# Kernel tuning notes

Hardware: AMD Instinct MI355X
Metric: run time of the kernel (lower is better)

## Reference

```python
import jax, jax.numpy as jnp
import numpy as np

B, S, D, H = 2, 2048, 1024, 16
HD = D // H
NEG = -10000.0


def setup_inputs() -> dict:
    key = jax.random.key(0)
    ks = jax.random.split(key, 9)
    # xavier-uniform-like scale for square d_model x d_model weights
    lim = float(np.sqrt(6.0 / (D + D)))
    mk_w = lambda k: jax.random.uniform(k, (D, D), jnp.float32, -lim, lim)
    return {
        "q": jax.random.normal(ks[0], (B, S, D), jnp.float32),
        "k": jax.random.normal(ks[1], (B, S, D), jnp.float32),
        "v": jax.random.normal(ks[2], (B, S, D), jnp.float32),
        "attn_mask": jax.random.randint(ks[3], (B, S), 0, 2, jnp.int32),
        "Wq": mk_w(ks[4]),
        "Wk": mk_w(ks[5]),
        "Wv": mk_w(ks[6]),
        "Wo": mk_w(ks[7]),
        "mask_future": 1,
    }


def reference(q, k, v, attn_mask, Wq, Wk, Wv, Wo, mask_future):
    # nn.Linear(bias=False): y = x @ W.T
    def split_heads(x, W):
        return (x @ W.T).reshape(B, S, H, HD).transpose(0, 2, 1, 3)  # [B,H,S,HD]

    qh = split_heads(q, Wq)
    kh = split_heads(k, Wk)
    vh = split_heads(v, Wv)

    scale = 1.0 / np.sqrt(HD)
    scores = jnp.einsum("bhld,bhsd->bhls", qh, kh) * scale  # [B,H,L,S]

    if mask_future:  # static python flag
        rows = jnp.arange(S)[:, None]
        cols = jnp.arange(S)[None, :]
        causal_bias = jnp.where(cols > rows, jnp.float32(NEG), jnp.float32(0.0))
        scores = scores + causal_bias

    # masked_fill(attn_mask == 0, -10000): sets score exactly to NEG (after bias add)
    pad = attn_mask[:, None, None, :]  # [B,1,1,S]
    scores = jnp.where(pad == 0, jnp.float32(NEG), scores)

    probs = jax.nn.softmax(scores, axis=-1)
    ctx = jnp.einsum("bhls,bhsd->bhld", probs, vh)  # [B,H,L,HD]
    ctx = ctx.transpose(0, 2, 1, 3).reshape(B, S, D)
    return ctx @ Wo.T
```

## Files before the change

kernel.cpp:

```cpp
#include <hip/hip_runtime.h>
#include <hip/hip_bf16.h>

typedef __attribute__((ext_vector_type(8))) short bf16x8;
typedef __attribute__((ext_vector_type(4))) short bf16x4;
typedef __attribute__((ext_vector_type(4))) float f32x4;

#define B_ 2
#define S_ 2048
#define D_ 1024
#define H_ 16
#define HD_ 64
#define M_ 4096
#define NEGV (-10000.0f)

#define NQ_ 4194304
#define NW_ 1048576

#if __has_builtin(__builtin_amdgcn_mfma_f32_16x16x16bf16_1k)
#define HAVE_MFMA16 1
#else
#define HAVE_MFMA16 0
#endif

static __device__ __forceinline__ unsigned short f2bf(float x) {
  __hip_bfloat16 h = __float2bfloat16(x);
  return *reinterpret_cast<unsigned short*>(&h);
}

static __device__ __forceinline__ bf16x8 cvt8(const float* p) {
  float4 a = *reinterpret_cast<const float4*>(p);
  float4 b = *reinterpret_cast<const float4*>(p + 4);
  bf16x8 r;
  r[0] = (short)f2bf(a.x); r[1] = (short)f2bf(a.y);
  r[2] = (short)f2bf(a.z); r[3] = (short)f2bf(a.w);
  r[4] = (short)f2bf(b.x); r[5] = (short)f2bf(b.y);
  r[6] = (short)f2bf(b.z); r[7] = (short)f2bf(b.w);
  return r;
}

static __device__ __forceinline__ void gl_lds16(const unsigned short* g, unsigned short* l) {
#if __has_builtin(__builtin_amdgcn_global_load_lds)
  __builtin_amdgcn_global_load_lds(
      (const __attribute__((address_space(1))) unsigned int*)g,
      (__attribute__((address_space(3))) unsigned int*)l, 16, 0, 0);
#else
  *reinterpret_cast<bf16x8*>(l) = *reinterpret_cast<const bf16x8*>(g);
#endif
}


__global__ __launch_bounds__(256) void cvt_all(const float* __restrict__ q,
                                               const float* __restrict__ k,
                                               const float* __restrict__ v,
                                               const float* __restrict__ wq,
                                               const float* __restrict__ wk,
                                               const float* __restrict__ wv,
                                               const float* __restrict__ wo,
                                               unsigned short* __restrict__ dst) {
  for (size_t c = (size_t)blockIdx.x * 256 + threadIdx.x; c < 2097152; c += (size_t)2048 * 256) {
    const size_t e = c * 8;
    const float* s;
    if (e < (size_t)NQ_)            s = q  + e;
    else if (e < (size_t)2 * NQ_)   s = k  + (e - (size_t)NQ_);
    else if (e < (size_t)3 * NQ_)   s = v  + (e - (size_t)2 * NQ_);
    else if (e < (size_t)3 * NQ_ + NW_)     s = wq + (e - (size_t)3 * NQ_);
    else if (e < (size_t)3 * NQ_ + 2 * NW_) s = wk + (e - (size_t)3 * NQ_ - NW_);
    else if (e < (size_t)3 * NQ_ + 3 * NW_) s = wv + (e - (size_t)3 * NQ_ - 2 * NW_);
    else                                    s = wo + (e - (size_t)3 * NQ_ - 3 * NW_);
    *reinterpret_cast<bf16x8*>(dst + e) = cvt8(s);
  }
}

template<bool HSPLIT>
static __device__ __forceinline__ void core_fast(const unsigned short* A,
                                                 const unsigned short* Bw,
                                                 unsigned short* Asm, unsigned short* Bsm,
                                                 int m0, int n0, f32x4 (*acc)[4]) {
  const int tid = threadIdx.x, lane = tid & 63, wid = tid >> 6;
  const int wm = wid >> 1, wn = wid & 1;
  const int l15 = lane & 15, l4 = lane >> 4;

  for (int k0 = 0; k0 < 1024; k0 += 64) {
    __syncthreads();
#pragma unroll
    for (int i = 0; i < 4; ++i) {
      const int idx = tid + 256 * i;
      const int row = idx >> 3;
      const int ce = ((idx & 7) * 8) ^ ((row & 7) << 3);
      const unsigned short* ga;
      if constexpr (HSPLIT) {
        const int m = m0 + row, kk = k0 + ce;
        const int bb = m >> 11, s = m & 2047;
        ga = A + (((size_t)(bb * H_ + (kk >> 6)) * S_ + s) * HD_ + (kk & 63));
      } else {
        ga = A + (size_t)(m0 + row) * 1024 + k0 + ce;
      }
      gl_lds16(ga, Asm + (size_t)idx * 8);
      gl_lds16(Bw + (size_t)(n0 + row) * 1024 + k0 + ce, Bsm + (size_t)idx * 8);
    }
    __syncthreads();
#pragma unroll
    for (int kk = 0; kk < 2; ++kk) {
      bf16x8 af[4], bfr[4];
#pragma unroll
      for (int f = 0; f < 4; ++f) {
        const int ra = wm * 64 + f * 16 + l15;
        const int ca = (kk * 32 + l4 * 8) ^ ((ra & 7) << 3);
        af[f] = *reinterpret_cast<const bf16x8*>(&Asm[ra * 64 + ca]);
        const int rb = wn * 64 + f * 16 + l15;
        const int cb = (kk * 32 + l4 * 8) ^ ((rb & 7) << 3);
        bfr[f] = *reinterpret_cast<const bf16x8*>(&Bsm[rb * 64 + cb]);
      }
#pragma unroll
      for (int fm = 0; fm < 4; ++fm)
#pragma unroll
        for (int fn = 0; fn < 4; ++fn)
          acc[fm][fn] = __builtin_amdgcn_mfma_f32_16x16x32_bf16(af[fm], bfr[fn], acc[fm][fn], 0, 0, 0);
    }
  }
}

__global__ __launch_bounds__(256) void gemm_qkv_fast(const unsigned short* __restrict__ qbf,
                                                     const unsigned short* __restrict__ kbf,
                                                     const unsigned short* __restrict__ vbf,
                                                     const unsigned short* __restrict__ wbf,
                                                     unsigned short* __restrict__ Qh,
                                                     unsigned short* __restrict__ Kh,
                                                     unsigned short* __restrict__ Vt) {
  __shared__ unsigned short Asm[128 * 64];
  __shared__ unsigned short Bsm[128 * 64];
  const int z = blockIdx.z;
  const unsigned short* A  = (z == 0) ? qbf : (z == 1) ? kbf : vbf;
  const unsigned short* Bw = wbf + (size_t)z * NW_;
  const int m0 = blockIdx.y * 128, n0 = blockIdx.x * 128;
  const int lane = threadIdx.x & 63, wid = threadIdx.x >> 6;
  const int wm = wid >> 1, wn = wid & 1;
  const int l15 = lane & 15, l4 = lane >> 4;
  f32x4 acc[4][4] = {};
  core_fast<false>(A, Bw, Asm, Bsm, m0, n0, acc);

#pragma unroll
  for (int fm = 0; fm < 4; ++fm) {
#pragma unroll
    for (int fn = 0; fn < 4; ++fn) {
      const int mg0 = m0 + wm * 64 + fm * 16 + l4 * 4;
      const int ng  = n0 + wn * 64 + fn * 16 + l15;
      const int bidx = mg0 >> 11, s = mg0 & 2047;
      const int h = ng >> 6, d = ng & 63;
      if (z < 2) {
        unsigned short* C = (z == 0) ? Qh : Kh;
#pragma unroll
        for (int r = 0; r < 4; ++r)
          C[((size_t)((bidx * H_ + h) * S_ + s + r)) * HD_ + d] = f2bf(acc[fm][fn][r]);
      } else {
        ushort4 pk;
        pk.x = f2bf(acc[fm][fn][0]); pk.y = f2bf(acc[fm][fn][1]);
        pk.z = f2bf(acc[fm][fn][2]); pk.w = f2bf(acc[fm][fn][3]);
        *reinterpret_cast<ushort4*>(&Vt[((size_t)((bidx * H_ + h) * HD_ + d)) * S_ + s]) = pk;
      }
    }
  }
}

__global__ __launch_bounds__(256) void gemm_o_fast(const unsigned short* __restrict__ ctx,
                                                   const unsigned short* __restrict__ wobf,
                                                   float* __restrict__ Cout) {
  __shared__ unsigned short Asm[128 * 64];
  __shared__ unsigned short Bsm[128 * 64];
  const int m0 = blockIdx.y * 128, n0 = blockIdx.x * 128;
  const int lane = threadIdx.x & 63, wid = threadIdx.x >> 6;
  const int wm = wid >> 1, wn = wid & 1;
  const int l15 = lane & 15, l4 = lane >> 4;
  f32x4 acc[4][4] = {};
  core_fast<true>(ctx, wobf, Asm, Bsm, m0, n0, acc);

#pragma unroll
  for (int fm = 0; fm < 4; ++fm)
#pragma unroll
    for (int fn = 0; fn < 4; ++fn) {
      const int mg0 = m0 + wm * 64 + fm * 16 + l4 * 4;
      const int ng  = n0 + wn * 64 + fn * 16 + l15;
#pragma unroll
      for (int r = 0; r < 4; ++r)
        Cout[(size_t)(mg0 + r) * 1024 + ng] = acc[fm][fn][r];
    }
}


template<bool AF32, bool BF32, bool HSPLIT>
static __device__ __forceinline__ void gemm_core(const void* Av, const void* Bv,
                                                 unsigned short* Asm, unsigned short* Bsm,
                                                 int m0, int n0, f32x4 (*acc)[4]) {
  constexpr int BK = 64, LDT = 72;
  constexpr int K = 1024;
  const int tid = threadIdx.x;
  const int lane = tid & 63, wid = tid >> 6;
  const int wm = wid >> 1, wn = wid & 1;
  const int l15 = lane & 15, l4 = lane >> 4;

  for (int k0 = 0; k0 < K; k0 += BK) {
    __syncthreads();
#pragma unroll
    for (int i = 0; i < 4; ++i) {
      int idx = tid + 256 * i;
      int row = idx >> 3, k8 = (idx & 7) * 8;
      bf16x8 va, vb;
      if constexpr (AF32) {
        va = cvt8((const float*)Av + (size_t)(m0 + row) * K + k0 + k8);
      } else if constexpr (HSPLIT) {
        const int m = m0 + row, kk = k0 + k8;
        const int bb = m >> 11, s = m & 2047;
        va = *reinterpret_cast<const bf16x8*>(
            (const unsigned short*)Av +
            (((size_t)(bb * H_ + (kk >> 6)) * S_ + s) * HD_ + (kk & 63)));
      } else {
        va = *reinterpret_cast<const bf16x8*>((const unsigned short*)Av + (size_t)(m0 + row) * K + k0 + k8);
      }
      if constexpr (BF32) {
        vb = cvt8((const float*)Bv + (size_t)(n0 + row) * K + k0 + k8);
      } else {
        vb = *reinterpret_cast<const bf16x8*>((const unsigned short*)Bv + (size_t)(n0 + row) * K + k0 + k8);
      }
      *reinterpret_cast<bf16x8*>(&Asm[row * LDT + k8]) = va;
      *reinterpret_cast<bf16x8*>(&Bsm[row * LDT + k8]) = vb;
    }
    __syncthreads();
#pragma unroll
    for (int kk = 0; kk < 2; ++kk) {
      bf16x8 af[4], bfr[4];
#pragma unroll
      for (int f = 0; f < 4; ++f) {
        af[f]  = *reinterpret_cast<const bf16x8*>(&Asm[(wm * 64 + f * 16 + l15) * LDT + kk * 32 + l4 * 8]);
        bfr[f] = *reinterpret_cast<const bf16x8*>(&Bsm[(wn * 64 + f * 16 + l15) * LDT + kk * 32 + l4 * 8]);
      }
#pragma unroll
      for (int fm = 0; fm < 4; ++fm)
#pragma unroll
        for (int fn = 0; fn < 4; ++fn)
          acc[fm][fn] = __builtin_amdgcn_mfma_f32_16x16x32_bf16(af[fm], bfr[fn], acc[fm][fn], 0, 0, 0);
    }
  }
}

__global__ __launch_bounds__(256) void gemm_qkv3(const float* __restrict__ q,
                                                 const float* __restrict__ k,
                                                 const float* __restrict__ v,
                                                 const float* __restrict__ Wq,
                                                 const float* __restrict__ Wk,
                                                 const float* __restrict__ Wv,
                                                 unsigned short* __restrict__ Qh,
                                                 unsigned short* __restrict__ Kh,
                                                 unsigned short* __restrict__ Vt) {
  constexpr int LDT = 72;
  __shared__ unsigned short Asm[128 * LDT];
  __shared__ unsigned short Bsm[128 * LDT];
  const int z = blockIdx.z;
  const float* A  = (z == 0) ? q  : (z == 1) ? k  : v;
  const float* Bw = (z == 0) ? Wq : (z == 1) ? Wk : Wv;
  const int m0 = blockIdx.y * 128, n0 = blockIdx.x * 128;
  const int lane = threadIdx.x & 63, wid = threadIdx.x >> 6;
  const int wm = wid >> 1, wn = wid & 1;
  const int l15 = lane & 15, l4 = lane >> 4;
  f32x4 acc[4][4] = {};
  gemm_core<true, true, false>(A, Bw, Asm, Bsm, m0, n0, acc);

#pragma unroll
  for (int fm = 0; fm < 4; ++fm) {
#pragma unroll
    for (int fn = 0; fn < 4; ++fn) {
      const int mg0 = m0 + wm * 64 + fm * 16 + l4 * 4;
      const int ng  = n0 + wn * 64 + fn * 16 + l15;
      const int bidx = mg0 >> 11, s = mg0 & 2047;
      const int h = ng >> 6, d = ng & 63;
      if (z < 2) {
        unsigned short* C = (z == 0) ? Qh : Kh;
#pragma unroll
        for (int r = 0; r < 4; ++r)
          C[((size_t)((bidx * H_ + h) * S_ + s + r)) * HD_ + d] = f2bf(acc[fm][fn][r]);
      } else {
        ushort4 pk;
        pk.x = f2bf(acc[fm][fn][0]); pk.y = f2bf(acc[fm][fn][1]);
        pk.z = f2bf(acc[fm][fn][2]); pk.w = f2bf(acc[fm][fn][3]);
        *reinterpret_cast<ushort4*>(&Vt[((size_t)((bidx * H_ + h) * HD_ + d)) * S_ + s]) = pk;
      }
    }
  }
}

__global__ __launch_bounds__(256) void gemm_oproj(const void* __restrict__ Av,
                                                  const void* __restrict__ Bv,
                                                  float* __restrict__ Cout) {
  constexpr int LDT = 72;
  __shared__ unsigned short Asm[128 * LDT];
  __shared__ unsigned short Bsm[128 * LDT];
  const int m0 = blockIdx.y * 128, n0 = blockIdx.x * 128;
  const int lane = threadIdx.x & 63, wid = threadIdx.x >> 6;
  const int wm = wid >> 1, wn = wid & 1;
  const int l15 = lane & 15, l4 = lane >> 4;
  f32x4 acc[4][4] = {};
  gemm_core<false, true, true>(Av, Bv, Asm, Bsm, m0, n0, acc);

#pragma unroll
  for (int fm = 0; fm < 4; ++fm)
#pragma unroll
    for (int fn = 0; fn < 4; ++fn) {
      const int mg0 = m0 + wm * 64 + fm * 16 + l4 * 4;
      const int ng  = n0 + wn * 64 + fn * 16 + l15;
#pragma unroll
      for (int r = 0; r < 4; ++r)
        Cout[(size_t)(mg0 + r) * 1024 + ng] = acc[fm][fn][r];
    }
}

__global__ __launch_bounds__(128) void attn_fwd(const unsigned short* Qh,
                                                const unsigned short* __restrict__ Kh,
                                                const unsigned short* __restrict__ Vt,
                                                const int* __restrict__ attn_mask,
                                                const int* __restrict__ mask_future,
                                                unsigned short* ctx) {
  constexpr int KVB = 64;
  __shared__ unsigned short Ksm[64 * 64];
  __shared__ unsigned short Vsm[64 * 64];
#if !HAVE_MFMA16
  __shared__ unsigned short Psm[2][16 * 72];
#endif
  __shared__ int s_any;
  const int tid = threadIdx.x, lane = tid & 63, wid = tid >> 6;
  const int l15 = lane & 15, l4 = lane >> 4;
  const int bh = blockIdx.y, b = bh >> 4;
  const int bx = (int)blockIdx.x;
  const bool causal = (mask_future[0] != 0);

  const unsigned short* Qb = Qh + (size_t)bh * S_ * HD_;
  const unsigned short* Kb = Kh + (size_t)bh * S_ * HD_;
  const unsigned short* Vb = Vt + (size_t)bh * HD_ * S_;
  const int* mrow = attn_mask + b * S_;

  for (int half = 0; half < 2; ++half) {
    const int q0 = (half ? (63 - bx) : bx) * 32;

    __syncthreads();
    if (tid == 0) s_any = 0;
    __syncthreads();
    for (int i = tid; i <= q0; i += 128)
      if (mrow[i]) s_any = 1;
    __syncthreads();
    const int kb_end = (causal && s_any) ? (q0 + 32) : S_;

    const int qrow = q0 + wid * 16 + l15;
    const bf16x8 qf0 = *reinterpret_cast<const bf16x8*>(&Qb[(size_t)qrow * HD_ + l4 * 8]);
    const bf16x8 qf1 = *reinterpret_cast<const bf16x8*>(&Qb[(size_t)qrow * HD_ + 32 + l4 * 8]);

    float m_run = -1e30f, l_run = 0.f;
    f32x4 o[4] = {};

    bf16x8 kreg[4], vreg[4];
#pragma unroll
    for (int j = 0; j < 4; ++j) {
      const int idx = tid + 128 * j;
      const int row = idx >> 3;
      const int ce = ((idx & 7) * 8) ^ ((row & 7) << 3);
      kreg[j] = *reinterpret_cast<const bf16x8*>(&Kb[(size_t)row * HD_ + ce]);
      vreg[j] = *reinterpret_cast<const bf16x8*>(&Vb[(size_t)row * S_ + ce]);
    }

    for (int kb = 0; kb < kb_end; kb += KVB) {
      __syncthreads();
#pragma unroll
      for (int j = 0; j < 4; ++j) {
        const int idx = tid + 128 * j;
        *reinterpret_cast<bf16x8*>(&Ksm[idx * 8]) = kreg[j];
        *reinterpret_cast<bf16x8*>(&Vsm[idx * 8]) = vreg[j];
      }
      __syncthreads();

      if (kb + KVB < kb_end) {
        const int kn = kb + KVB;
#pragma unroll
        for (int j = 0; j < 4; ++j) {
          const int idx = tid + 128 * j;
          const int row = idx >> 3;
          const int ce = ((idx & 7) * 8) ^ ((row & 7) << 3);
          kreg[j] = *reinterpret_cast<const bf16x8*>(&Kb[(size_t)(kn + row) * HD_ + ce]);
          vreg[j] = *reinterpret_cast<const bf16x8*>(&Vb[(size_t)row * S_ + kn + ce]);
        }
      }

      f32x4 sc[4];
#pragma unroll
      for (int nf = 0; nf < 4; ++nf) {
        const int ra = nf * 16 + l15, sw = (ra & 7) << 3;
        bf16x8 kf0 = *reinterpret_cast<const bf16x8*>(&Ksm[ra * 64 + ((l4 * 8) ^ sw)]);
        bf16x8 kf1 = *reinterpret_cast<const bf16x8*>(&Ksm[ra * 64 + ((32 + l4 * 8) ^ sw)]);
        f32x4 z = {};
        z = __builtin_amdgcn_mfma_f32_16x16x32_bf16(kf0, qf0, z, 0, 0, 0);
        z = __builtin_amdgcn_mfma_f32_16x16x32_bf16(kf1, qf1, z, 0, 0, 0);
        sc[nf] = z;
      }

      float p[4][4];
      float mx = -1e30f;
#pragma unroll
      for (int nf = 0; nf < 4; ++nf) {
        const int4 mk4 = *reinterpret_cast<const int4*>(&mrow[kb + nf * 16 + l4 * 4]);
        const int kbase = kb + nf * 16 + l4 * 4;
#pragma unroll
        for (int r = 0; r < 4; ++r) {
          float vv = sc[nf][r] * 0.125f;
          if (causal && (kbase + r) > qrow) vv += NEGV;
          const int mkr = (r == 0) ? mk4.x : (r == 1) ? mk4.y : (r == 2) ? mk4.z : mk4.w;
          if (mkr == 0) vv = NEGV;
          p[nf][r] = vv;
          mx = fmaxf(mx, vv);
        }
      }
      mx = fmaxf(mx, __shfl_xor(mx, 16));
      mx = fmaxf(mx, __shfl_xor(mx, 32));
      const float m_new = fmaxf(m_run, mx);
      const float scale = __expf(m_run - m_new);
      float s_loc = 0.f;
#pragma unroll
      for (int nf = 0; nf < 4; ++nf)
#pragma unroll
        for (int r = 0; r < 4; ++r) {
          float e = __expf(p[nf][r] - m_new);
          p[nf][r] = e;
          s_loc += e;
        }
      s_loc += __shfl_xor(s_loc, 16);
      s_loc += __shfl_xor(s_loc, 32);
      l_run = l_run * scale + s_loc;
      m_run = m_new;

      float sq[4];
#pragma unroll
      for (int r = 0; r < 4; ++r) sq[r] = __shfl(scale, l4 * 4 + r);
#pragma unroll
      for (int nf2 = 0; nf2 < 4; ++nf2)
#pragma unroll
        for (int r = 0; r < 4; ++r) o[nf2][r] *= sq[r];

#if HAVE_MFMA16
      bf16x4 pk[4];
#pragma unroll
      for (int nf = 0; nf < 4; ++nf) {
        bf16x4 t;
        t[0] = (short)f2bf(p[nf][0]); t[1] = (short)f2bf(p[nf][1]);
        t[2] = (short)f2bf(p[nf][2]); t[3] = (short)f2bf(p[nf][3]);
        pk[nf] = t;
      }
#pragma unroll
      for (int nf2 = 0; nf2 < 4; ++nf2) {
        const int rv = nf2 * 16 + l15, swv = (rv & 7) << 3;
#pragma unroll
        for (int nf = 0; nf < 4; ++nf) {
          bf16x4 vf = *reinterpret_cast<const bf16x4*>(&Vsm[rv * 64 + ((nf * 16 + l4 * 4) ^ swv)]);
          o[nf2] = __builtin_amdgcn_mfma_f32_16x16x16bf16_1k(pk[nf], vf, o[nf2], 0, 0, 0);
        }
      }
#else
      unsigned short* Pw = &Psm[wid][0];
#pragma unroll
      for (int nf = 0; nf < 4; ++nf)
#pragma unroll
        for (int r = 0; r < 4; ++r)
          Pw[l15 * 72 + nf * 16 + l4 * 4 + r] = f2bf(p[nf][r]);
#pragma unroll
      for (int nf2 = 0; nf2 < 4; ++nf2) {
        const int rv = nf2 * 16 + l15, swv = (rv & 7) << 3;
#pragma unroll
        for (int kk = 0; kk < 2; ++kk) {
          bf16x8 pf = *reinterpret_cast<const bf16x8*>(&Pw[l15 * 72 + kk * 32 + l4 * 8]);
          bf16x8 vf = *reinterpret_cast<const bf16x8*>(&Vsm[rv * 64 + ((kk * 32 + l4 * 8) ^ swv)]);
          o[nf2] = __builtin_amdgcn_mfma_f32_16x16x32_bf16(pf, vf, o[nf2], 0, 0, 0);
        }
      }
#endif
    }

    const float linv = 1.f / l_run;
    float lq[4];
#pragma unroll
    for (int r = 0; r < 4; ++r) lq[r] = __shfl(linv, l4 * 4 + r);
#pragma unroll
    for (int nf2 = 0; nf2 < 4; ++nf2)
#pragma unroll
      for (int r = 0; r < 4; ++r) {
        const int rowg = q0 + wid * 16 + l4 * 4 + r;
        ctx[((size_t)bh * S_ + rowg) * HD_ + nf2 * 16 + l15] = f2bf(o[nf2][r] * lq[r]);
      }
  }
}

extern "C" void kernel_launch(void* const* d_in, const int* in_sizes, int n_in,
                              void* d_out, int out_size, void* d_ws, size_t ws_size,
                              hipStream_t stream) {
  const float* q = (const float*)d_in[0];
  const float* k = (const float*)d_in[1];
  const float* v = (const float*)d_in[2];
  const int* attn_mask = (const int*)d_in[3];
  const float* Wq = (const float*)d_in[4];
  const float* Wk = (const float*)d_in[5];
  const float* Wv = (const float*)d_in[6];
  const float* Wo = (const float*)d_in[7];
  const int* mask_future = (const int*)d_in[8];

  unsigned short* ws = (unsigned short*)d_ws;
  unsigned short* Vt = (unsigned short*)d_out;
  float* out = (float*)d_out;
  (void)in_sizes; (void)n_in; (void)out_size;

  const size_t CVT_ELEMS = (size_t)3 * NQ_ + 4 * NW_;
  const size_t NEED = (CVT_ELEMS + 2 * (size_t)NQ_) * 2;

  if (ws_size >= NEED) {
    unsigned short* cvt = ws;
    unsigned short* qbf = cvt;
    unsigned short* kbf = cvt + (size_t)NQ_;
    unsigned short* vbf = cvt + (size_t)2 * NQ_;
    unsigned short* wbf = cvt + (size_t)3 * NQ_;
    unsigned short* Qh  = cvt + CVT_ELEMS;
    unsigned short* Kh  = Qh + (size_t)NQ_;

    cvt_all<<<2048, 256, 0, stream>>>(q, k, v, Wq, Wk, Wv, Wo, cvt);
    gemm_qkv_fast<<<dim3(8, 32, 3), 256, 0, stream>>>(qbf, kbf, vbf, wbf, Qh, Kh, Vt);
    attn_fwd<<<dim3(32, 32), 128, 0, stream>>>(Qh, Kh, Vt, attn_mask, mask_future, Qh);
    gemm_o_fast<<<dim3(8, 32), 256, 0, stream>>>(Qh, wbf + (size_t)3 * NW_, out);
  } else {
    unsigned short* Qh = ws;
    unsigned short* Kh = ws + (size_t)NQ_;
    gemm_qkv3<<<dim3(8, 32, 3), 256, 0, stream>>>(q, k, v, Wq, Wk, Wv, Qh, Kh, Vt);
    attn_fwd<<<dim3(32, 32), 128, 0, stream>>>(Qh, Kh, Vt, attn_mask, mask_future, Qh);
    gemm_oproj<<<dim3(8, 32), 256, 0, stream>>>(Qh, Wo, out);
  }
}
```

Before: 212.7 us.

## Split attention into single-wave blocks of 16 query rows, longest-first order

The attention kernel now launches 4096 one-wave blocks, each handling 16 query rows for one (batch, head). Blocks are ordered so the longest causal tiles are scheduled first, replacing the old pairing of two 32-row halves per 128-thread block. With a single wave per block, all __syncthreads and the shared mask flag go away, and the padding check uses a wave-wide __any. The trade-off is that each K/V tile is now loaded and staged per 16 query rows instead of 32, which doubles K/V reads from L2. Each lane also holds twice as many prefetch registers.

```diff
diff --git a/kernel.cpp b/kernel.cpp
--- a/kernel.cpp
+++ b/kernel.cpp
@@ -312,184 +312,179 @@
     }
 }
 
-__global__ __launch_bounds__(128) void attn_fwd(const unsigned short* Qh,
-                                                const unsigned short* __restrict__ Kh,
-                                                const unsigned short* __restrict__ Vt,
-                                                const int* __restrict__ attn_mask,
-                                                const int* __restrict__ mask_future,
-                                                unsigned short* ctx) {
+__global__ __launch_bounds__(64) void attn_fwd(const unsigned short* Qh,
+                                               const unsigned short* __restrict__ Kh,
+                                               const unsigned short* __restrict__ Vt,
+                                               const int* __restrict__ attn_mask,
+                                               const int* __restrict__ mask_future,
+                                               unsigned short* ctx) {
   constexpr int KVB = 64;
   __shared__ unsigned short Ksm[64 * 64];
   __shared__ unsigned short Vsm[64 * 64];
-#if !HAVE_MFMA16
-  __shared__ unsigned short Psm[2][16 * 72];
-#endif
-  __shared__ int s_any;
-  const int tid = threadIdx.x, lane = tid & 63, wid = tid >> 6;
-  const int l15 = lane & 15, l4 = lane >> 4;
-  const int bh = blockIdx.y, b = bh >> 4;
+  const int lane = threadIdx.x & 63;
+  const int l15 = lane & 15, l4 = lane >> 4;
   const int bx = (int)blockIdx.x;
+  const int tile = 127 - (bx >> 5);
+  const int bh = bx & 31, b = bh >> 4;
+  const int q0 = tile * 16;
   const bool causal = (mask_future[0] != 0);
+  const int* mrow = attn_mask + b * S_;
+
+  int anyv = 0;
+  for (int i = lane; i <= q0; i += 64) anyv |= mrow[i];
+  const int kb_end = (causal && __any(anyv)) ? (q0 + 16) : S_;
 
   const unsigned short* Qb = Qh + (size_t)bh * S_ * HD_;
   const unsigned short* Kb = Kh + (size_t)bh * S_ * HD_;
   const unsigned short* Vb = Vt + (size_t)bh * HD_ * S_;
-  const int* mrow = attn_mask + b * S_;
-
-  for (int half = 0; half < 2; ++half) {
-    const int q0 = (half ? (63 - bx) : bx) * 32;
-
-    __syncthreads();
-    if (tid == 0) s_any = 0;
-    __syncthreads();
-    for (int i = tid; i <= q0; i += 128)
-      if (mrow[i]) s_any = 1;
-    __syncthreads();
-    const int kb_end = (causal && s_any) ? (q0 + 32) : S_;
-
-    const int qrow = q0 + wid * 16 + l15;
-    const bf16x8 qf0 = *reinterpret_cast<const bf16x8*>(&Qb[(size_t)qrow * HD_ + l4 * 8]);
-    const bf16x8 qf1 = *reinterpret_cast<const bf16x8*>(&Qb[(size_t)qrow * HD_ + 32 + l4 * 8]);
-
-    float m_run = -1e30f, l_run = 0.f;
-    f32x4 o[4] = {};
-
-    bf16x8 kreg[4], vreg[4];
-#pragma unroll
-    for (int j = 0; j < 4; ++j) {
-      const int idx = tid + 128 * j;
-      const int row = idx >> 3;
-      const int ce = ((idx & 7) * 8) ^ ((row & 7) << 3);
-      kreg[j] = *reinterpret_cast<const bf16x8*>(&Kb[(size_t)row * HD_ + ce]);
-      vreg[j] = *reinterpret_cast<const bf16x8*>(&Vb[(size_t)row * S_ + ce]);
-    }
-
-    for (int kb = 0; kb < kb_end; kb += KVB) {
-      __syncthreads();
-#pragma unroll
-      for (int j = 0; j < 4; ++j) {
-        const int idx = tid + 128 * j;
-        *reinterpret_cast<bf16x8*>(&Ksm[idx * 8]) = kreg[j];
-        *reinterpret_cast<bf16x8*>(&Vsm[idx * 8]) = vreg[j];
-      }
-      __syncthreads();
-
-      if (kb + KVB < kb_end) {
-        const int kn = kb + KVB;
-#pragma unroll
-        for (int j = 0; j < 4; ++j) {
-          const int idx = tid + 128 * j;
-          const int row = idx >> 3;
-          const int ce = ((idx & 7) * 8) ^ ((row & 7) << 3);
-          kreg[j] = *reinterpret_cast<const bf16x8*>(&Kb[(size_t)(kn + row) * HD_ + ce]);
-          vreg[j] = *reinterpret_cast<const bf16x8*>(&Vb[(size_t)row * S_ + kn + ce]);
+
+  const int qrow = q0 + l15;
+  const bf16x8 qf0 = *reinterpret_cast<const bf16x8*>(&Qb[(size_t)qrow * HD_ + l4 * 8]);
+  const bf16x8 qf1 = *reinterpret_cast<const bf16x8*>(&Qb[(size_t)qrow * HD_ + 32 + l4 * 8]);
+
+  float m_run = -1e30f, l_run = 0.f;
+  f32x4 o[4] = {};
+
+  bf16x8 kreg[8], vreg[8];
+#pragma unroll
+  for (int j = 0; j < 8; ++j) {
+    const int idx = lane + 64 * j;
+    const int row = idx >> 3;
+    const int ce = ((idx & 7) * 8) ^ ((row & 7) << 3);
+    kreg[j] = *reinterpret_cast<const bf16x8*>(&Kb[(size_t)row * HD_ + ce]);
+    vreg[j] = *reinterpret_cast<const bf16x8*>(&Vb[(size_t)row * S_ + ce]);
+  }
+
+  for (int kb = 0; kb < kb_end; kb += KVB) {
+#pragma unroll
+    for (int j = 0; j < 8; ++j) {
+      const int idx = lane + 64 * j;
+      *reinterpret_cast<bf16x8*>(&Ksm[idx * 8]) = kreg[j];
+      *reinterpret_cast<bf16x8*>(&Vsm[idx * 8]) = vreg[j];
+    }
+
+    if (kb + KVB < kb_end) {
+      const int kn = kb + KVB;
+#pragma unroll
+      for (int j = 0; j < 8; ++j) {
+        const int idx = lane + 64 * j;
+        const int row = idx >> 3;
+        const int ce = ((idx & 7) * 8) ^ ((row & 7) << 3);
+        kreg[j] = *reinterpret_cast<const bf16x8*>(&Kb[(size_t)(kn + row) * HD_ + ce]);
+        vreg[j] = *reinterpret_cast<const bf16x8*>(&Vb[(size_t)row * S_ + kn + ce]);
+      }
+    }
+
+    f32x4 sc[4];
+#pragma unroll
+    for (int nf = 0; nf < 4; ++nf) {
+      const int ra = nf * 16 + l15, sw = (ra & 7) << 3;
+      bf16x8 kf0 = *reinterpret_cast<const bf16x8*>(&Ksm[ra * 64 + ((l4 * 8) ^ sw)]);
+      bf16x8 kf1 = *reinterpret_cast<const bf16x8*>(&Ksm[ra * 64 + ((32 + l4 * 8) ^ sw)]);
+      f32x4 z = {};
+      z = __builtin_amdgcn_mfma_f32_16x16x32_bf16(kf0, qf0, z, 0, 0, 0);
+      z = __builtin_amdgcn_mfma_f32_16x16x32_bf16(kf1, qf1, z, 0, 0, 0);
+      sc[nf] = z;
+    }
+
+    float p[4][4];
+    float mx = -1e30f;
+#pragma unroll
+    for (int nf = 0; nf < 4; ++nf) {
+      const int4 mk4 = *reinterpret_cast<const int4*>(&mrow[kb + nf * 16 + l4 * 4]);
+      const int kbase = kb + nf * 16 + l4 * 4;
+#pragma unroll
+      for (int r = 0; r < 4; ++r) {
+        float vv = sc[nf][r] * 0.125f;
+        if (causal && (kbase + r) > qrow) vv += NEGV;
+        const int mkr = (r == 0) ? mk4.x : (r == 1) ? mk4.y : (r == 2) ? mk4.z : mk4.w;
+        if (mkr == 0) vv = NEGV;
+        p[nf][r] = vv;
+        mx = fmaxf(mx, vv);
+      }
+    }
+    mx = fmaxf(mx, __shfl_xor(mx, 16));
+    mx = fmaxf(mx, __shfl_xor(mx, 32));
+    const float m_new = fmaxf(m_run, mx);
+    const float scale = __expf(m_run - m_new);
+    float s_loc = 0.f;
+#pragma unroll
+    for (int nf = 0; nf < 4; ++nf)
+#pragma unroll
+      for (int r = 0; r < 4; ++r) {
+        float e = __expf(p[nf][r] - m_new);
+        p[nf][r] = e;
+        s_loc += e;
+      }
+    s_loc += __shfl_xor(s_loc, 16);
+    s_loc += __shfl_xor(s_loc, 32);
+    l_run = l_run * scale + s_loc;
+    m_run = m_new;
+
+    float sq[4];
+#pragma unroll
+    for (int r = 0; r < 4; ++r) sq[r] = __shfl(scale, l4 * 4 + r);
+#pragma unroll
+    for (int nf2 = 0; nf2 < 4; ++nf2)
+#pragma unroll
+      for (int r = 0; r < 4; ++r) o[nf2][r] *= sq[r];
+
+#if HAVE_MFMA16
+    bf16x4 pk[4];
+#pragma unroll
+    for (int nf = 0; nf < 4; ++nf) {
+      bf16x4 t;
+      t[0] = (short)f2bf(p[nf][0]); t[1] = (short)f2bf(p[nf][1]);
+      t[2] = (short)f2bf(p[nf][2]); t[3] = (short)f2bf(p[nf][3]);
+      pk[nf] = t;
+    }
+#pragma unroll
+    for (int nf2 = 0; nf2 < 4; ++nf2) {
+      const int rv = nf2 * 16 + l15, swv = (rv & 7) << 3;
+#pragma unroll
+      for (int nf = 0; nf < 4; ++nf) {
+        bf16x4 vf = *reinterpret_cast<const bf16x4*>(&Vsm[rv * 64 + ((nf * 16 + l4 * 4) ^ swv)]);
+        o[nf2] = __builtin_amdgcn_mfma_f32_16x16x16bf16_1k(pk[nf], vf, o[nf2], 0, 0, 0);
+      }
+    }
+#else
+    bf16x4 pk[4];
+#pragma unroll
+    for (int nf = 0; nf < 4; ++nf) {
+      bf16x4 t;
+      t[0] = (short)f2bf(p[nf][0]); t[1] = (short)f2bf(p[nf][1]);
+      t[2] = (short)f2bf(p[nf][2]); t[3] = (short)f2bf(p[nf][3]);
+      pk[nf] = t;
+    }
+#pragma unroll
+    for (int nf2 = 0; nf2 < 4; ++nf2) {
+      const int rv = nf2 * 16 + l15, swv = (rv & 7) << 3;
+#pragma unroll
+      for (int nf = 0; nf < 4; ++nf) {
+        bf16x4 vf = *reinterpret_cast<const bf16x4*>(&Vsm[rv * 64 + ((nf * 16 + l4 * 4) ^ swv)]);
+#pragma unroll
+        for (int r = 0; r < 4; ++r) {
+          float pv = p[nf][r];
+          float vvv = (float)(((unsigned int)(unsigned short)vf[r]) << 16 ? 0.f : 0.f);
+          (void)vvv; (void)pv;
         }
-      }
-
-      f32x4 sc[4];
-#pragma unroll
-      for (int nf = 0; nf < 4; ++nf) {
-        const int ra = nf * 16 + l15, sw = (ra & 7) << 3;
-        bf16x8 kf0 = *reinterpret_cast<const bf16x8*>(&Ksm[ra * 64 + ((l4 * 8) ^ sw)]);
-        bf16x8 kf1 = *reinterpret_cast<const bf16x8*>(&Ksm[ra * 64 + ((32 + l4 * 8) ^ sw)]);
-        f32x4 z = {};
-        z = __builtin_amdgcn_mfma_f32_16x16x32_bf16(kf0, qf0, z, 0, 0, 0);
-        z = __builtin_amdgcn_mfma_f32_16x16x32_bf16(kf1, qf1, z, 0, 0, 0);
-        sc[nf] = z;
-      }
-
-      float p[4][4];
-      float mx = -1e30f;
-#pragma unroll
-      for (int nf = 0; nf < 4; ++nf) {
-        const int4 mk4 = *reinterpret_cast<const int4*>(&mrow[kb + nf * 16 + l4 * 4]);
-        const int kbase = kb + nf * 16 + l4 * 4;
-#pragma unroll
-        for (int r = 0; r < 4; ++r) {
-          float vv = sc[nf][r] * 0.125f;
-          if (causal && (kbase + r) > qrow) vv += NEGV;
-          const int mkr = (r == 0) ? mk4.x : (r == 1) ? mk4.y : (r == 2) ? mk4.z : mk4.w;
-          if (mkr == 0) vv = NEGV;
-          p[nf][r] = vv;
-          mx = fmaxf(mx, vv);
-        }
-      }
-      mx = fmaxf(mx, __shfl_xor(mx, 16));
-      mx = fmaxf(mx, __shfl_xor(mx, 32));
-      const float m_new = fmaxf(m_run, mx);
-      const float scale = __expf(m_run - m_new);
-      float s_loc = 0.f;
-#pragma unroll
-      for (int nf = 0; nf < 4; ++nf)
-#pragma unroll
-        for (int r = 0; r < 4; ++r) {
-          float e = __expf(p[nf][r] - m_new);
-          p[nf][r] = e;
-          s_loc += e;
-        }
-      s_loc += __shfl_xor(s_loc, 16);
-      s_loc += __shfl_xor(s_loc, 32);
-      l_run = l_run * scale + s_loc;
-      m_run = m_new;
-
-      float sq[4];
-#pragma unroll
-      for (int r = 0; r < 4; ++r) sq[r] = __shfl(scale, l4 * 4 + r);
-#pragma unroll
-      for (int nf2 = 0; nf2 < 4; ++nf2)
-#pragma unroll
-        for (int r = 0; r < 4; ++r) o[nf2][r] *= sq[r];
-
-#if HAVE_MFMA16
-      bf16x4 pk[4];
-#pragma unroll
-      for (int nf = 0; nf < 4; ++nf) {
-        bf16x4 t;
-        t[0] = (short)f2bf(p[nf][0]); t[1] = (short)f2bf(p[nf][1]);
-        t[2] = (short)f2bf(p[nf][2]); t[3] = (short)f2bf(p[nf][3]);
-        pk[nf] = t;
-      }
-#pragma unroll
-      for (int nf2 = 0; nf2 < 4; ++nf2) {
-        const int rv = nf2 * 16 + l15, swv = (rv & 7) << 3;
-#pragma unroll
-        for (int nf = 0; nf < 4; ++nf) {
-          bf16x4 vf = *reinterpret_cast<const bf16x4*>(&Vsm[rv * 64 + ((nf * 16 + l4 * 4) ^ swv)]);
-          o[nf2] = __builtin_amdgcn_mfma_f32_16x16x16bf16_1k(pk[nf], vf, o[nf2], 0, 0, 0);
-        }
-      }
-#else
-      unsigned short* Pw = &Psm[wid][0];
-#pragma unroll
-      for (int nf = 0; nf < 4; ++nf)
-#pragma unroll
-        for (int r = 0; r < 4; ++r)
-          Pw[l15 * 72 + nf * 16 + l4 * 4 + r] = f2bf(p[nf][r]);
-#pragma unroll
-      for (int nf2 = 0; nf2 < 4; ++nf2) {
-        const int rv = nf2 * 16 + l15, swv = (rv & 7) << 3;
-#pragma unroll
-        for (int kk = 0; kk < 2; ++kk) {
-          bf16x8 pf = *reinterpret_cast<const bf16x8*>(&Pw[l15 * 72 + kk * 32 + l4 * 8]);
-          bf16x8 vf = *reinterpret_cast<const bf16x8*>(&Vsm[rv * 64 + ((kk * 32 + l4 * 8) ^ swv)]);
-          o[nf2] = __builtin_amdgcn_mfma_f32_16x16x32_bf16(pf, vf, o[nf2], 0, 0, 0);
-        }
-      }
+        o[nf2] = __builtin_amdgcn_mfma_f32_16x16x16bf16_1k(pk[nf], vf, o[nf2], 0, 0, 0);
+      }
+    }
 #endif
-    }
-
-    const float linv = 1.f / l_run;
-    float lq[4];
-#pragma unroll
-    for (int r = 0; r < 4; ++r) lq[r] = __shfl(linv, l4 * 4 + r);
-#pragma unroll
-    for (int nf2 = 0; nf2 < 4; ++nf2)
-#pragma unroll
-      for (int r = 0; r < 4; ++r) {
-        const int rowg = q0 + wid * 16 + l4 * 4 + r;
-        ctx[((size_t)bh * S_ + rowg) * HD_ + nf2 * 16 + l15] = f2bf(o[nf2][r] * lq[r]);
-      }
-  }
+  }
+
+  const float linv = 1.f / l_run;
+  float lq[4];
+#pragma unroll
+  for (int r = 0; r < 4; ++r) lq[r] = __shfl(linv, l4 * 4 + r);
+#pragma unroll
+  for (int nf2 = 0; nf2 < 4; ++nf2)
+#pragma unroll
+    for (int r = 0; r < 4; ++r) {
+      const int rowg = q0 + l4 * 4 + r;
+      ctx[((size_t)bh * S_ + rowg) * HD_ + nf2 * 16 + l15] = f2bf(o[nf2][r] * lq[r]);
+    }
 }
 
 extern "C" void kernel_launch(void* const* d_in, const int* in_sizes, int n_in,
@@ -524,13 +519,13 @@
 
     cvt_all<<<2048, 256, 0, stream>>>(q, k, v, Wq, Wk, Wv, Wo, cvt);
     gemm_qkv_fast<<<dim3(8, 32, 3), 256, 0, stream>>>(qbf, kbf, vbf, wbf, Qh, Kh, Vt);
-    attn_fwd<<<dim3(32, 32), 128, 0, stream>>>(Qh, Kh, Vt, attn_mask, mask_future, Qh);
+    attn_fwd<<<4096, 64, 0, stream>>>(Qh, Kh, Vt, attn_mask, mask_future, Qh);
     gemm_o_fast<<<dim3(8, 32), 256, 0, stream>>>(Qh, wbf + (size_t)3 * NW_, out);
   } else {
     unsigned short* Qh = ws;
     unsigned short* Kh = ws + (size_t)NQ_;
     gemm_qkv3<<<dim3(8, 32, 3), 256, 0, stream>>>(q, k, v, Wq, Wk, Wv, Qh, Kh, Vt);
-    attn_fwd<<<dim3(32, 32), 128, 0, stream>>>(Qh, Kh, Vt, attn_mask, mask_future, Qh);
+    attn_fwd<<<4096, 64, 0, stream>>>(Qh, Kh, Vt, attn_mask, mask_future, Qh);
     gemm_oproj<<<dim3(8, 32), 256, 0, stream>>>(Qh, Wo, out);
   }
 }
```

After: 193.6 us. 9.0% less time.

## Process 64 query rows per block with two fragments per warp

Applied to the files above, without the earlier changes.

Each attention block now owns one 64-row query tile, with each warp holding two 16-row Q fragments, instead of two paired 32-row tiles. Every K/V tile staged in shared memory is therefore reused by twice as many query rows, and the padding-mask loads are hoisted out of the per-fragment loop. To spread the uneven causal work, a tile is picked with a swizzle of blockIdx.x and blockIdx.y in place of the old front/back pairing. The trade-off is higher register pressure from doubled accumulators, and per-block work now varies with the causal tile position.

```diff
diff --git a/kernel.cpp b/kernel.cpp
--- a/kernel.cpp
+++ b/kernel.cpp
@@ -328,64 +328,72 @@
   const int tid = threadIdx.x, lane = tid & 63, wid = tid >> 6;
   const int l15 = lane & 15, l4 = lane >> 4;
   const int bh = blockIdx.y, b = bh >> 4;
-  const int bx = (int)blockIdx.x;
+  const int q0 = (int)((blockIdx.x + 9 * blockIdx.y) & 31) * 64;
   const bool causal = (mask_future[0] != 0);
+  const int* mrow = attn_mask + b * S_;
+
+  if (tid == 0) s_any = 0;
+  __syncthreads();
+  for (int i = tid; i <= q0; i += 128)
+    if (mrow[i]) s_any = 1;
+  __syncthreads();
+  const int kb_end = (causal && s_any) ? (q0 + 64) : S_;
 
   const unsigned short* Qb = Qh + (size_t)bh * S_ * HD_;
   const unsigned short* Kb = Kh + (size_t)bh * S_ * HD_;
   const unsigned short* Vb = Vt + (size_t)bh * HD_ * S_;
-  const int* mrow = attn_mask + b * S_;
-
-  for (int half = 0; half < 2; ++half) {
-    const int q0 = (half ? (63 - bx) : bx) * 32;
-
+
+  int qrow[2];
+  bf16x8 qf0[2], qf1[2];
+#pragma unroll
+  for (int f = 0; f < 2; ++f) {
+    qrow[f] = q0 + wid * 32 + f * 16 + l15;
+    qf0[f] = *reinterpret_cast<const bf16x8*>(&Qb[(size_t)qrow[f] * HD_ + l4 * 8]);
+    qf1[f] = *reinterpret_cast<const bf16x8*>(&Qb[(size_t)qrow[f] * HD_ + 32 + l4 * 8]);
+  }
+
+  float m_run[2] = {-1e30f, -1e30f}, l_run[2] = {0.f, 0.f};
+  f32x4 o[2][4] = {};
+
+  bf16x8 kreg[4], vreg[4];
+#pragma unroll
+  for (int j = 0; j < 4; ++j) {
+    const int idx = tid + 128 * j;
+    const int row = idx >> 3;
+    const int ce = ((idx & 7) * 8) ^ ((row & 7) << 3);
+    kreg[j] = *reinterpret_cast<const bf16x8*>(&Kb[(size_t)row * HD_ + ce]);
+    vreg[j] = *reinterpret_cast<const bf16x8*>(&Vb[(size_t)row * S_ + ce]);
+  }
+
+  for (int kb = 0; kb < kb_end; kb += KVB) {
     __syncthreads();
-    if (tid == 0) s_any = 0;
-    __syncthreads();
-    for (int i = tid; i <= q0; i += 128)
-      if (mrow[i]) s_any = 1;
-    __syncthreads();
-    const int kb_end = (causal && s_any) ? (q0 + 32) : S_;
-
-    const int qrow = q0 + wid * 16 + l15;
-    const bf16x8 qf0 = *reinterpret_cast<const bf16x8*>(&Qb[(size_t)qrow * HD_ + l4 * 8]);
-    const bf16x8 qf1 = *reinterpret_cast<const bf16x8*>(&Qb[(size_t)qrow * HD_ + 32 + l4 * 8]);
-
-    float m_run = -1e30f, l_run = 0.f;
-    f32x4 o[4] = {};
-
-    bf16x8 kreg[4], vreg[4];
 #pragma unroll
     for (int j = 0; j < 4; ++j) {
       const int idx = tid + 128 * j;
-      const int row = idx >> 3;
-      const int ce = ((idx & 7) * 8) ^ ((row & 7) << 3);
-      kreg[j] = *reinterpret_cast<const bf16x8*>(&Kb[(size_t)row * HD_ + ce]);
-      vreg[j] = *reinterpret_cast<const bf16x8*>(&Vb[(size_t)row * S_ + ce]);
-    }
-
-    for (int kb = 0; kb < kb_end; kb += KVB) {
-      __syncthreads();
+      *reinterpret_cast<bf16x8*>(&Ksm[idx * 8]) = kreg[j];
+      *reinterpret_cast<bf16x8*>(&Vsm[idx * 8]) = vreg[j];
+    }
+    __syncthreads();
+
+    if (kb + KVB < kb_end) {
+      const int kn = kb + KVB;
 #pragma unroll
       for (int j = 0; j < 4; ++j) {
         const int idx = tid + 128 * j;
-        *reinterpret_cast<bf16x8*>(&Ksm[idx * 8]) = kreg[j];
-        *reinterpret_cast<bf16x8*>(&Vsm[idx * 8]) = vreg[j];
-      }
-      __syncthreads();
-
-      if (kb + KVB < kb_end) {
-        const int kn = kb + KVB;
-#pragma unroll
-        for (int j = 0; j < 4; ++j) {
-          const int idx = tid + 128 * j;
-          const int row = idx >> 3;
-          const int ce = ((idx & 7) * 8) ^ ((row & 7) << 3);
-          kreg[j] = *reinterpret_cast<const bf16x8*>(&Kb[(size_t)(kn + row) * HD_ + ce]);
-          vreg[j] = *reinterpret_cast<const bf16x8*>(&Vb[(size_t)row * S_ + kn + ce]);
-        }
-      }
-
+        const int row = idx >> 3;
+        const int ce = ((idx & 7) * 8) ^ ((row & 7) << 3);
+        kreg[j] = *reinterpret_cast<const bf16x8*>(&Kb[(size_t)(kn + row) * HD_ + ce]);
+        vreg[j] = *reinterpret_cast<const bf16x8*>(&Vb[(size_t)row * S_ + kn + ce]);
+      }
+    }
+
+    int4 mk4 [4];
+#pragma unroll
+    for (int nf = 0; nf < 4; ++nf)
+      mk4[nf] = *reinterpret_cast<const int4*>(&mrow[kb + nf * 16 + l4 * 4]);
+
+#pragma unroll
+    for (int f = 0; f < 2; ++f) {
       f32x4 sc[4];
 #pragma unroll
       for (int nf = 0; nf < 4; ++nf) {
@@ -393,8 +401,8 @@
         bf16x8 kf0 = *reinterpret_cast<const bf16x8*>(&Ksm[ra * 64 + ((l4 * 8) ^ sw)]);
         bf16x8 kf1 = *reinterpret_cast<const bf16x8*>(&Ksm[ra * 64 + ((32 + l4 * 8) ^ sw)]);
         f32x4 z = {};
-        z = __builtin_amdgcn_mfma_f32_16x16x32_bf16(kf0, qf0, z, 0, 0, 0);
-        z = __builtin_amdgcn_mfma_f32_16x16x32_bf16(kf1, qf1, z, 0, 0, 0);
+        z = __builtin_amdgcn_mfma_f32_16x16x32_bf16(kf0, qf0[f], z, 0, 0, 0);
+        z = __builtin_amdgcn_mfma_f32_16x16x32_bf16(kf1, qf1[f], z, 0, 0, 0);
         sc[nf] = z;
       }
 
@@ -402,13 +410,12 @@
       float mx = -1e30f;
 #pragma unroll
       for (int nf = 0; nf < 4; ++nf) {
-        const int4 mk4 = *reinterpret_cast<const int4*>(&mrow[kb + nf * 16 + l4 * 4]);
         const int kbase = kb + nf * 16 + l4 * 4;
 #pragma unroll
         for (int r = 0; r < 4; ++r) {
           float vv = sc[nf][r] * 0.125f;
-          if (causal && (kbase + r) > qrow) vv += NEGV;
-          const int mkr = (r == 0) ? mk4.x : (r == 1) ? mk4.y : (r == 2) ? mk4.z : mk4.w;
+          if (causal && (kbase + r) > qrow[f]) vv += NEGV;
+          const int mkr = (r == 0) ? mk4[nf].x : (r == 1) ? mk4[nf].y : (r == 2) ? mk4[nf].z : mk4[nf].w;
           if (mkr == 0) vv = NEGV;
           p[nf][r] = vv;
           mx = fmaxf(mx, vv);
@@ -416,8 +423,8 @@
       }
       mx = fmaxf(mx, __shfl_xor(mx, 16));
       mx = fmaxf(mx, __shfl_xor(mx, 32));
-      const float m_new = fmaxf(m_run, mx);
-      const float scale = __expf(m_run - m_new);
+      const float m_new = fmaxf(m_run[f], mx);
+      const float scale = __expf(m_run[f] - m_new);
       float s_loc = 0.f;
 #pragma unroll
       for (int nf = 0; nf < 4; ++nf)
@@ -429,8 +436,8 @@
         }
       s_loc += __shfl_xor(s_loc, 16);
       s_loc += __shfl_xor(s_loc, 32);
-      l_run = l_run * scale + s_loc;
-      m_run = m_new;
+      l_run[f] = l_run[f] * scale + s_loc;
+      m_run[f] = m_new;
 
       float sq[4];
 #pragma unroll
@@ -438,7 +445,7 @@
 #pragma unroll
       for (int nf2 = 0; nf2 < 4; ++nf2)
 #pragma unroll
-        for (int r = 0; r < 4; ++r) o[nf2][r] *= sq[r];
+        for (int r = 0; r < 4; ++r) o[f][nf2][r] *= sq[r];
 
 #if HAVE_MFMA16
       bf16x4 pk[4];
@@ -455,7 +462,7 @@
 #pragma unroll
         for (int nf = 0; nf < 4; ++nf) {
           bf16x4 vf = *reinterpret_cast<const bf16x4*>(&Vsm[rv * 64 + ((nf * 16 + l4 * 4) ^ swv)]);
-          o[nf2] = __builtin_amdgcn_mfma_f32_16x16x16bf16_1k(pk[nf], vf, o[nf2], 0, 0, 0);
+          o[f][nf2] = __builtin_amdgcn_mfma_f32_16x16x16bf16_1k(pk[nf], vf, o[f][nf2], 0, 0, 0);
         }
       }
 #else
@@ -472,13 +479,16 @@
         for (int kk = 0; kk < 2; ++kk) {
           bf16x8 pf = *reinterpret_cast<const bf16x8*>(&Pw[l15 * 72 + kk * 32 + l4 * 8]);
           bf16x8 vf = *reinterpret_cast<const bf16x8*>(&Vsm[rv * 64 + ((kk * 32 + l4 * 8) ^ swv)]);
-          o[nf2] = __builtin_amdgcn_mfma_f32_16x16x32_bf16(pf, vf, o[nf2], 0, 0, 0);
+          o[f][nf2] = __builtin_amdgcn_mfma_f32_16x16x32_bf16(pf, vf, o[f][nf2], 0, 0, 0);
         }
       }
 #endif
     }
-
-    const float linv = 1.f / l_run;
+  }
+
+#pragma unroll
+  for (int f = 0; f < 2; ++f) {
+    const float linv = 1.f / l_run[f];
     float lq[4];
 #pragma unroll
     for (int r = 0; r < 4; ++r) lq[r] = __shfl(linv, l4 * 4 + r);
@@ -486,8 +496,8 @@
     for (int nf2 = 0; nf2 < 4; ++nf2)
 #pragma unroll
       for (int r = 0; r < 4; ++r) {
-        const int rowg = q0 + wid * 16 + l4 * 4 + r;
-        ctx[((size_t)bh * S_ + rowg) * HD_ + nf2 * 16 + l15] = f2bf(o[nf2][r] * lq[r]);
+        const int rowg = q0 + wid * 32 + f * 16 + l4 * 4 + r;
+        ctx[((size_t)bh * S_ + rowg) * HD_ + nf2 * 16 + l15] = f2bf(o[f][nf2][r] * lq[r]);
       }
   }
 }
```

New measurement: 176.5 us. 17.0% less time.
